# Kernel tuning notes

Hardware: AMD Instinct MI355X
Metric: run time of the kernel (lower is better)

The kernel has to match this reference:

```python
import jax, jax.numpy as jnp
import numpy as np

T = 16384      # trajectory length
Z = 8          # num_zones
DIN = 8        # person_attrs_dim
E = 16         # num edges
PENALTY = 1000.0
DIFFUSION_STRENGTH = 0.2
EPS = 1e-20


def setup_inputs() -> dict:
    key = jax.random.key(0)
    ks = jax.random.split(key, 20)
    s = 0.05  # weight scale
    return {
        "person_attrs": jax.random.normal(ks[0], (DIN,), jnp.float32),
        "times": jnp.arange(T, dtype=jnp.float32),
        "gumbel_u": jax.random.uniform(ks[1], (T, Z), jnp.float32),
        "edge_index": jax.random.randint(ks[2], (2, E), 0, Z),
        "W1": jax.random.normal(ks[3], (256, DIN + 1 + Z), jnp.float32) * s,
        "b1": jnp.zeros((256,), jnp.float32),
        "W2": jax.random.normal(ks[4], (128, 256), jnp.float32) * s,
        "b2": jnp.zeros((128,), jnp.float32),
        "W3": jax.random.normal(ks[5], (64, 128), jnp.float32) * s,
        "b3": jnp.zeros((64,), jnp.float32),
        "W4": jax.random.normal(ks[6], (Z, 64), jnp.float32) * s,
        "b4": jnp.zeros((Z,), jnp.float32),
        "D1": jax.random.normal(ks[7], (128, DIN + 1), jnp.float32) * s,
        "d1": jnp.zeros((128,), jnp.float32),
        "D2": jax.random.normal(ks[8], (64, 128), jnp.float32) * s,
        "d2": jnp.zeros((64,), jnp.float32),
        "D3": jax.random.normal(ks[9], (Z, 64), jnp.float32) * s,
        "d3": jnp.zeros((Z,), jnp.float32),
        "tau": jnp.asarray(1.0, jnp.float32),
    }


def _adjacency(edge_index, num_zones):
    A = jnp.zeros((num_zones, num_zones), jnp.float32)
    A = A.at[edge_index[0], edge_index[1]].set(1.0)
    A = A.at[edge_index[1], edge_index[0]].set(1.0)
    d = jnp.arange(num_zones)
    return A.at[d, d].set(1.0)


def _forward(person_attrs, times, gumbel_u, W1, b1, W2, b2, W3, b3, W4, b4,
             D1, d1, D2, d2, D3, d3, tau, edge_index):
    num_zones = W4.shape[0]
    din = person_attrs.shape[0]
    A = _adjacency(edge_index, num_zones)

    # normalized time: times / times[-1] if times[-1] > 0 else 0
    last = times[-1]
    denom = jnp.where(last > 0, last, jnp.asarray(1.0, times.dtype))
    norm_t = jnp.where(last > 0, times / denom, jnp.zeros_like(times))  # [T]

    # Precompute (attrs, time)-dependent parts batched over all timesteps.
    # trajectory_net layer 1 split: columns [0:din]=attrs, [din]=time, [din+1:]=zone one-hot
    f_base = person_attrs @ W1[:, :din].T + norm_t[:, None] * W1[:, din][None, :] + b1  # [T,256]
    W1z = W1[:, din + 1:]  # [256, Z]

    # diversity_net depends only on (attrs, time): batch it fully.
    h = jax.nn.relu(person_attrs @ D1[:, :din].T + norm_t[:, None] * D1[:, din][None, :] + d1)  # [T,128]
    h = jax.nn.relu(h @ D2.T + d2)                                                              # [T,64]
    diversity = jnp.tanh(h @ D3.T + d3)                                                         # [T,Z]

    gumbels = -jnp.log(-jnp.log(gumbel_u + EPS) + EPS)  # [T,Z]

    zone0 = jax.nn.one_hot(0, num_zones, dtype=jnp.float32)

    def step(zone_soft, xs):
        f1, dv, g = xs
        h1 = jax.nn.relu(f1 + W1z @ zone_soft)
        h2 = jax.nn.relu(W2 @ h1 + b2)
        h3 = jax.nn.relu(W3 @ h2 + b3)
        base_logits = W4 @ h3 + b4
        combined = base_logits + DIFFUSION_STRENGTH * dv
        cur = jnp.argmax(zone_soft)
        constrained = combined - PENALTY * (1.0 - A[cur])
        y = jax.nn.softmax((constrained + g) / tau)
        nxt = jnp.argmax(y)
        hard = jax.nn.one_hot(nxt, num_zones, dtype=y.dtype)
        zone_next = y + jax.lax.stop_gradient(hard - y)  # straight-through hard gumbel
        return zone_next, (constrained, nxt)

    _, (traj_logits, traj_zones) = jax.lax.scan(step, zone0, (f_base, diversity, gumbels))
    return traj_logits, traj_zones


def reference(person_attrs, times, gumbel_u, edge_index, W1, b1, W2, b2, W3, b3,
              W4, b4, D1, d1, D2, d2, D3, d3, tau):
    return _forward(person_attrs, times, gumbel_u, W1, b1, W2, b2, W3, b3, W4, b4,
                    D1, d1, D2, d2, D3, d3, tau, edge_index)
```

## Files before the change

kernel.cpp:

```cpp
#include <hip/hip_runtime.h>
#include <cstdint>

#define T_STEPS 16384

#define WS_U     0
#define WS_V     256
#define WS_W1ZT  512
#define WS_PEN   2560
#define WS_A     2624
#define WS_W4T   2688
#define WS_W2T   3968
#define WS_W3T   36736
#define WS_DV    53120
#define WS_G     184192
#define WS_CONS  315264
#define WS_ABT   1363840
#define WS_A4LR  1888128
#define WS_H3LR  1920896
#define WS_END_F 2183040
#define WSB_NXT8 ((size_t)WS_END_F * 4)
#define WSB_CUR  (WSB_NXT8 + 131072)
#define WSB_CRX  (WSB_CUR + 65536)

#define PB_DIV   0
#define PB_W2T   256
#define PB_W3T   (PB_W2T + 128)
#define PB_GUM   (PB_W3T + 32)
#define PB_SETUP (PB_GUM + 512)
#define NB_PREP  (PB_SETUP + 1)

__device__ __forceinline__ unsigned int fn_compose(unsigned int hi, unsigned int lo) {
  unsigned int r = 0;
  #pragma unroll
  for (int x = 0; x < 8; ++x) {
    unsigned int m = (lo >> (3 * x)) & 7u;
    r |= ((hi >> (3 * m)) & 7u) << (3 * x);
  }
  return r;
}

__global__ void __launch_bounds__(256) k_prepdiv(
    const float* __restrict__ pa, const float* __restrict__ times,
    const float* __restrict__ gum, const int* __restrict__ edge,
    const float* __restrict__ W1, const float* __restrict__ b1,
    const float* __restrict__ W2, const float* __restrict__ W3,
    const float* __restrict__ W4,
    const float* __restrict__ D1, const float* __restrict__ d1,
    const float* __restrict__ D2, const float* __restrict__ d2,
    const float* __restrict__ D3, const float* __restrict__ d3,
    float* __restrict__ ws) {
  __shared__ float sD2[64 * 128];
  __shared__ float sudc[128], svdc[128];
  __shared__ float part[3][8][64];
  int b = blockIdx.x, tid = threadIdx.x;
  if (b < PB_W2T) {
    int lane = tid & 63;
    int w = __builtin_amdgcn_readfirstlane(tid >> 6);
    int t = b * 64 + lane;
    float last = times[T_STEPS - 1];
    float st = (last > 0.0f) ? times[t] / last : 0.0f;
    #pragma unroll
    for (int i = 0; i < 8; ++i)
      ((float4*)sD2)[i * 256 + tid] = ((const float4*)D2)[i * 256 + tid];
    if (tid < 128) {
      float acc = d1[tid];
      #pragma unroll
      for (int i = 0; i < 8; ++i) acc = fmaf(pa[i], D1[tid * 9 + i], acc);
      sudc[tid] = acc;
      svdc[tid] = D1[tid * 9 + 8];
    }
    __syncthreads();
    int j0 = __builtin_amdgcn_readfirstlane(w * 16);
    float accj[16];
    #pragma unroll
    for (int jj = 0; jj < 16; ++jj) accj[jj] = d2[j0 + jj];
    #pragma unroll 4
    for (int k = 0; k < 128; ++k) {
      float h1 = fmaxf(fmaf(st, svdc[k], sudc[k]), 0.0f);
      #pragma unroll
      for (int jj = 0; jj < 16; ++jj)
        accj[jj] = fmaf(sD2[(j0 + jj) * 128 + k], h1, accj[jj]);
    }
    float dvp[8];
    #pragma unroll
    for (int z = 0; z < 8; ++z) dvp[z] = (w == 0) ? d3[z] : 0.0f;
    #pragma unroll
    for (int jj = 0; jj < 16; ++jj) {
      float h2 = fmaxf(accj[jj], 0.0f);
      #pragma unroll
      for (int z = 0; z < 8; ++z)
        dvp[z] = fmaf(D3[z * 64 + j0 + jj], h2, dvp[z]);
    }
    if (w > 0) {
      #pragma unroll
      for (int z = 0; z < 8; ++z) part[w - 1][z][lane] = dvp[z];
    }
    __syncthreads();
    if (w == 0) {
      #pragma unroll
      for (int z = 0; z < 8; ++z) {
        float dvv = dvp[z] + part[0][z][lane] + part[1][z][lane] + part[2][z][lane];
        ws[WS_DV + t * 8 + z] = tanhf(dvv);
      }
    }
  } else if (b < PB_W3T) {
    int e = (b - PB_W2T) * 256 + tid;
    int k = e >> 7, j = e & 127;
    ws[WS_W2T + e] = W2[j * 256 + k];
  } else if (b < PB_GUM) {
    int e = (b - PB_W3T) * 256 + tid;
    int i = e & 63, j = e >> 6;
    ws[WS_W3T + e] = W3[i * 128 + j];
  } else if (b < PB_SETUP) {
    int e = (b - PB_GUM) * 256 + tid;
    float uu = gum[e];
    ws[WS_G + e] = -logf(-logf(uu + 1e-20f) + 1e-20f);
  } else {
    {
      int k = tid;
      float acc = b1[k];
      #pragma unroll
      for (int i = 0; i < 8; ++i) acc = fmaf(pa[i], W1[k * 17 + i], acc);
      ws[WS_U + k] = acc;
      ws[WS_V + k] = W1[k * 17 + 8];
    }
    for (int e = tid; e < 2048; e += 256) {
      int cc = e >> 8, k = e & 255;
      ws[WS_W1ZT + e] = W1[k * 17 + 9 + cc];
    }
    for (int e = tid; e < 512; e += 256) {
      int k = e >> 3, z = e & 7;
      ws[WS_W4T + e] = W4[z * 64 + k];
    }
    if (tid < 64) ws[WS_A + tid] = ((tid >> 3) == (tid & 7)) ? 1.0f : 0.0f;
    __syncthreads();
    if (tid == 0) {
      for (int e = 0; e < 16; ++e) {
        int aa = edge[e], bb = edge[16 + e];
        ws[WS_A + aa * 8 + bb] = 1.0f;
        ws[WS_A + bb * 8 + aa] = 1.0f;
      }
    }
    __syncthreads();
    if (tid < 64) ws[WS_PEN + tid] = 1000.0f * (1.0f - ws[WS_A + tid]);
  }
}

__global__ void __launch_bounds__(256) k_ab4(
    const float* __restrict__ times,
    const float* __restrict__ u_, const float* __restrict__ v_,
    const float* __restrict__ w1zt, const float* __restrict__ w2t,
    const float* __restrict__ w3t, const float* __restrict__ w4t,
    const float* __restrict__ b2, const float* __restrict__ b3,
    const float* __restrict__ b4,
    float* __restrict__ abt, int* __restrict__ crx,
    float* __restrict__ a4lr, float* __restrict__ h3lr) {
  __shared__ float s_au[256], s_av[256];
  __shared__ float s_pa[128], s_pb[128];
  __shared__ unsigned long long s_bal[4];
  __shared__ float s_h2L[128], s_h2R[128];
  __shared__ float s_h3pL[4][64], s_h3pR[4][64];
  __shared__ float s_h3L[64], s_h3R[64];
  __shared__ int s_d2, s_d3, s_cnt;
  int blk = blockIdx.x;
  int c = blk >> 8, tile = blk & 255;
  int tid = threadIdx.x;
  float last = times[T_STEPS - 1];
  float stL = (last > 0.0f) ? times[tile * 64] / last : 0.0f;
  float stR = (last > 0.0f) ? times[tile * 64 + 63] / last : 0.0f;
  {
    float uk = u_[tid] + w1zt[c * 256 + tid];
    float vk = v_[tid];
    float valL = fmaf(stL, vk, uk);
    float valR = fmaf(stR, vk, uk);
    float mn = fminf(valL, valR);
    float mx = fmaxf(valL, valR);
    bool act = (mn > 0.0f);
    bool cross = (!act) && (mx > 0.0f);
    s_au[tid] = act ? uk : 0.0f;
    s_av[tid] = act ? vk : 0.0f;
    unsigned long long bal = __ballot(cross);
    if ((tid & 63) == 0) s_bal[tid >> 6] = bal;
  }
  if (tid == 0) { s_d2 = 0; s_d3 = 0; }
  __syncthreads();
  if (tid == 0) {
    int cnt = 0;
    int list8[8];
    #pragma unroll
    for (int i = 0; i < 8; ++i) list8[i] = 0;
    #pragma unroll
    for (int w = 0; w < 4; ++w) {
      unsigned long long m = s_bal[w];
      while (m) {
        int bit = __ffsll(m) - 1;
        if (cnt < 8) list8[cnt] = w * 64 + bit;
        ++cnt;
        m &= (m - 1);
      }
    }
    crx[blk * 12] = cnt;
    s_cnt = cnt;
    #pragma unroll
    for (int i = 0; i < 8; ++i) crx[blk * 12 + 1 + i] = list8[i];
  }
  {
    int j = tid & 127, half = tid >> 7;
    float A = 0.0f, B = 0.0f;
    const float* wrow = w2t + half * 128 * 128 + j;
    int kb = half * 128;
    #pragma unroll 4
    for (int kk = 0; kk < 128; ++kk) {
      float w = wrow[kk * 128];
      A = fmaf(s_au[kb + kk], w, A);
      B = fmaf(s_av[kb + kk], w, B);
    }
    if (half == 1) { s_pa[j] = A; s_pb[j] = B; }
    __syncthreads();
    if (half == 0) {
      float Af = A + s_pa[j] + b2[j];
      float Bf = B + s_pb[j];
      abt[(size_t)blk * 256 + j * 2]     = Af;
      abt[(size_t)blk * 256 + j * 2 + 1] = Bf;
      float preL = fmaf(stL, Bf, Af);
      float preR = fmaf(stR, Bf, Af);
      if ((preL > 0.0f) != (preR > 0.0f)) atomicOr(&s_d2, 1);
      s_h2L[j] = fmaxf(preL, 0.0f);
      s_h2R[j] = fmaxf(preR, 0.0f);
    }
  }
  __syncthreads();
  {
    int i = tid & 63, jq = tid >> 6;
    float aL = (jq == 0) ? b3[i] : 0.0f;
    float aR = aL;
    int j0 = jq * 32;
    #pragma unroll 4
    for (int jj = 0; jj < 32; ++jj) {
      float w = w3t[(j0 + jj) * 64 + i];
      aL = fmaf(w, s_h2L[j0 + jj], aL);
      aR = fmaf(w, s_h2R[j0 + jj], aR);
    }
    s_h3pL[jq][i] = aL;
    s_h3pR[jq][i] = aR;
  }
  __syncthreads();
  if (tid < 64) {
    float preL = s_h3pL[0][tid] + s_h3pL[1][tid] + s_h3pL[2][tid] + s_h3pL[3][tid];
    float preR = s_h3pR[0][tid] + s_h3pR[1][tid] + s_h3pR[2][tid] + s_h3pR[3][tid];
    if ((preL > 0.0f) != (preR > 0.0f)) atomicOr(&s_d3, 1);
    s_h3L[tid] = fmaxf(preL, 0.0f);
    s_h3R[tid] = fmaxf(preR, 0.0f);
    h3lr[(size_t)blk * 128 + tid]      = preL;
    h3lr[(size_t)blk * 128 + 64 + tid] = preR;
  }
  __syncthreads();
  if (tid < 8) {
    float aL = b4[tid], aR = b4[tid];
    #pragma unroll 8
    for (int i = 0; i < 64; ++i) {
      float w = w4t[i * 8 + tid];
      aL = fmaf(w, s_h3L[i], aL);
      aR = fmaf(w, s_h3R[i], aR);
    }
    a4lr[blk * 16 + tid]     = aL;
    a4lr[blk * 16 + 8 + tid] = aR;
  }
  if (tid == 0) {
    int flag = 0;
    if (s_cnt == 0 && s_d2 == 0) flag = s_d3 ? 2 : 1;
    crx[blk * 12 + 9] = flag;
  }
}

__global__ void __launch_bounds__(256, 8) k_mlp(
    const float* __restrict__ times,
    const float* __restrict__ u_, const float* __restrict__ v_,
    const float* __restrict__ w1zt, const float* __restrict__ w2t,
    const float* __restrict__ abt, const int* __restrict__ crx,
    const float* __restrict__ a4lr, const float* __restrict__ h3lr,
    const float* __restrict__ w3t, const float* __restrict__ w4t,
    const float* __restrict__ b2, const float* __restrict__ b3,
    const float* __restrict__ b4,
    const float* __restrict__ dv, const float* __restrict__ gt,
    const float* __restrict__ pen, const float* __restrict__ tau,
    float* __restrict__ cons_out, unsigned char* __restrict__ nxt_out) {
  __shared__ float part[3][8][64];
  int tid = threadIdx.x;
  int lane = tid & 63;
  int iq = __builtin_amdgcn_readfirstlane(tid >> 6);
  int blk = blockIdx.x;
  int c = blk >> 8, tgrp = blk & 255;
  int t = tgrp * 64 + lane;
  int abase = blk * 256;
  int cbase = blk * 12;
  int flag = crx[cbase + 9];

  if (flag == 1) {
    if (iq == 0) {
      float frac = (float)lane * (1.0f / 63.0f);
      float a4[8];
      #pragma unroll
      for (int z = 0; z < 8; ++z) {
        float L = a4lr[blk * 16 + z];
        float R = a4lr[blk * 16 + 8 + z];
        a4[z] = fmaf(frac, R - L, L);
      }
      float4 dv0 = *(const float4*)(dv + (size_t)t * 8);
      float4 dv1 = *(const float4*)(dv + (size_t)t * 8 + 4);
      float4 g0  = *(const float4*)(gt + (size_t)t * 8);
      float4 g1  = *(const float4*)(gt + (size_t)t * 8 + 4);
      float dvv[8] = {dv0.x, dv0.y, dv0.z, dv0.w, dv1.x, dv1.y, dv1.z, dv1.w};
      float gv[8]  = {g0.x, g0.y, g0.z, g0.w, g1.x, g1.y, g1.z, g1.w};
      float sgn = (tau[0] > 0.0f) ? 1.0f : -1.0f;
      float cons[8];
      float best = 0.0f; int bz = 0;
      #pragma unroll
      for (int z = 0; z < 8; ++z) {
        float lg = fmaf(0.2f, dvv[z], a4[z]) - pen[c * 8 + z];
        cons[z] = lg;
        float yv = (lg + gv[z]) * sgn;
        if (z == 0) { best = yv; bz = 0; }
        else if (yv > best) { best = yv; bz = z; }
      }
      float* co = cons_out + ((size_t)t * 8 + c) * 8;
      *(float4*)co = make_float4(cons[0], cons[1], cons[2], cons[3]);
      *(float4*)(co + 4) = make_float4(cons[4], cons[5], cons[6], cons[7]);
      nxt_out[t * 8 + c] = (unsigned char)bz;
    }
    return;
  }

  float last = times[T_STEPS - 1];
  float st = (last > 0.0f) ? times[t] / last : 0.0f;
  const float* w1c = w1zt + c * 256;
  int cnt = crx[cbase];

  float acc[16];
  if (flag == 2) {
    float frac = (float)lane * (1.0f / 63.0f);
    #pragma unroll
    for (int i = 0; i < 16; ++i) {
      float L = h3lr[(size_t)blk * 128 + iq * 16 + i];
      float R = h3lr[(size_t)blk * 128 + 64 + iq * 16 + i];
      acc[i] = fmaf(frac, R - L, L);
    }
  } else {
    #pragma unroll
    for (int i = 0; i < 16; ++i) acc[i] = b3[iq * 16 + i];
    const float* w3 = w3t + iq * 16;

    if (cnt == 0) {
      #pragma unroll 4
      for (int j = 0; j < 128; ++j) {
        float A = abt[abase + j * 2];
        float B = abt[abase + j * 2 + 1];
        float h2 = fmaxf(fmaf(st, B, A), 0.0f);
        #pragma unroll
        for (int i = 0; i < 16; ++i)
          acc[i] = fmaf(w3[j * 64 + i], h2, acc[i]);
      }
    } else if (cnt <= 8) {
      int kk[8];
      #pragma unroll
      for (int i = 0; i < 8; ++i) kk[i] = (i < cnt) ? crx[cbase + 1 + i] : 0;
      float hx[8];
      #pragma unroll
      for (int i = 0; i < 8; ++i)
        hx[i] = (i < cnt) ? fmaxf(fmaf(st, v_[kk[i]], u_[kk[i]] + w1c[kk[i]]), 0.0f) : 0.0f;
      #pragma unroll 2
      for (int j = 0; j < 128; ++j) {
        float A = abt[abase + j * 2];
        float B = abt[abase + j * 2 + 1];
        float h2p = fmaf(st, B, A);
        #pragma unroll
        for (int i = 0; i < 8; ++i)
          h2p = fmaf(hx[i], w2t[kk[i] * 128 + j], h2p);
        float h2 = fmaxf(h2p, 0.0f);
        #pragma unroll
        for (int i = 0; i < 16; ++i)
          acc[i] = fmaf(w3[j * 64 + i], h2, acc[i]);
      }
    } else {
      for (int j = 0; j < 128; ++j) {
        float h2p = b2[j];
        for (int k = 0; k < 256; ++k) {
          float h1 = fmaxf(fmaf(st, v_[k], u_[k] + w1c[k]), 0.0f);
          h2p = fmaf(w2t[k * 128 + j], h1, h2p);
        }
        float h2 = fmaxf(h2p, 0.0f);
        #pragma unroll
        for (int i = 0; i < 16; ++i)
          acc[i] = fmaf(w3[j * 64 + i], h2, acc[i]);
      }
    }
  }

  float p[8];
  #pragma unroll
  for (int z = 0; z < 8; ++z) p[z] = (iq == 0) ? b4[z] : 0.0f;
  #pragma unroll 4
  for (int i = 0; i < 16; ++i) {
    float h3 = fmaxf(acc[i], 0.0f);
    #pragma unroll
    for (int z = 0; z < 8; ++z)
      p[z] = fmaf(w4t[(iq * 16 + i) * 8 + z], h3, p[z]);
  }
  if (iq > 0) {
    #pragma unroll
    for (int z = 0; z < 8; ++z) part[iq - 1][z][lane] = p[z];
  }
  __syncthreads();
  if (iq == 0) {
    float a4[8];
    #pragma unroll
    for (int z = 0; z < 8; ++z)
      a4[z] = p[z] + part[0][z][lane] + part[1][z][lane] + part[2][z][lane];
    float4 dv0 = *(const float4*)(dv + (size_t)t * 8);
    float4 dv1 = *(const float4*)(dv + (size_t)t * 8 + 4);
    float4 g0  = *(const float4*)(gt + (size_t)t * 8);
    float4 g1  = *(const float4*)(gt + (size_t)t * 8 + 4);
    float dvv[8] = {dv0.x, dv0.y, dv0.z, dv0.w, dv1.x, dv1.y, dv1.z, dv1.w};
    float gv[8]  = {g0.x, g0.y, g0.z, g0.w, g1.x, g1.y, g1.z, g1.w};
    float sgn = (tau[0] > 0.0f) ? 1.0f : -1.0f;
    float cons[8];
    float best = 0.0f; int bz = 0;
    #pragma unroll
    for (int z = 0; z < 8; ++z) {
      float lg = fmaf(0.2f, dvv[z], a4[z]) - pen[c * 8 + z];
      cons[z] = lg;
      float yv = (lg + gv[z]) * sgn;
      if (z == 0) { best = yv; bz = 0; }
      else if (yv > best) { best = yv; bz = z; }
    }
    float* co = cons_out + ((size_t)t * 8 + c) * 8;
    *(float4*)co = make_float4(cons[0], cons[1], cons[2], cons[3]);
    *(float4*)(co + 4) = make_float4(cons[4], cons[5], cons[6], cons[7]);
    nxt_out[t * 8 + c] = (unsigned char)bz;
  }
}

__global__ void __launch_bounds__(1024) k_phaseC(float* __restrict__ ws, float* __restrict__ d_out) {
  int tid = threadIdx.x;
  const unsigned char* nxt8 = (const unsigned char*)ws + WSB_NXT8;
  unsigned int* cur_arr = (unsigned int*)((char*)ws + WSB_CUR);
  const unsigned int IDENT = 0x00FAC688u;
  unsigned int f[16];
  int t0 = tid * 16;
  unsigned int F = IDENT;
  #pragma unroll
  for (int i = 0; i < 16; ++i) {
    uint2 b = *(const uint2*)(nxt8 + (size_t)(t0 + i) * 8);
    unsigned int fn = 0;
    #pragma unroll
    for (int q = 0; q < 4; ++q) fn |= ((b.x >> (8 * q)) & 7u) << (3 * q);
    #pragma unroll
    for (int q = 0; q < 4; ++q) fn |= ((b.y >> (8 * q)) & 7u) << (3 * (q + 4));
    f[i] = fn;
    F = fn_compose(fn, F);
  }
  __shared__ unsigned int sc[1024];
  sc[tid] = F;
  __syncthreads();
  #pragma unroll
  for (int d = 1; d < 1024; d <<= 1) {
    unsigned int v = sc[tid];
    unsigned int p = (tid >= d) ? sc[tid - d] : 0u;
    unsigned int nv = (tid >= d) ? fn_compose(v, p) : v;
    __syncthreads();
    sc[tid] = nv;
    __syncthreads();
  }
  unsigned int E = (tid == 0) ? IDENT : sc[tid - 1];
  unsigned int state = E & 7u;
  #pragma unroll
  for (int i = 0; i < 16; ++i) {
    int tt = t0 + i;
    cur_arr[tt] = state;
    unsigned int nx = (f[i] >> (3 * state)) & 7u;
    d_out[131072 + tt] = (float)nx;
    state = nx;
  }
}

__global__ void k_gather(const float* __restrict__ ws, float* __restrict__ d_out) {
  int idx = blockIdx.x * 256 + threadIdx.x;
  const unsigned int* cur_arr = (const unsigned int*)((const char*)ws + WSB_CUR);
  int t = idx >> 3, z = idx & 7;
  unsigned int cur = cur_arr[t];
  d_out[idx] = ws[WS_CONS + (t * 8 + (int)cur) * 8 + z];
}

extern "C" void kernel_launch(void* const* d_in, const int* in_sizes, int n_in,
                              void* d_out, int out_size, void* d_ws, size_t ws_size,
                              hipStream_t stream) {
  const float* pa    = (const float*)d_in[0];
  const float* times = (const float*)d_in[1];
  const float* gum   = (const float*)d_in[2];
  const int*   edge  = (const int*)d_in[3];
  const float* W1  = (const float*)d_in[4];
  const float* b1  = (const float*)d_in[5];
  const float* W2  = (const float*)d_in[6];
  const float* b2  = (const float*)d_in[7];
  const float* W3  = (const float*)d_in[8];
  const float* b3  = (const float*)d_in[9];
  const float* W4  = (const float*)d_in[10];
  const float* b4  = (const float*)d_in[11];
  const float* D1  = (const float*)d_in[12];
  const float* d1v = (const float*)d_in[13];
  const float* D2  = (const float*)d_in[14];
  const float* d2v = (const float*)d_in[15];
  const float* D3  = (const float*)d_in[16];
  const float* d3v = (const float*)d_in[17];
  const float* tau = (const float*)d_in[18];
  float* ws = (float*)d_ws;
  float* out = (float*)d_out;
  int* crx = (int*)((char*)d_ws + WSB_CRX);

  k_prepdiv<<<NB_PREP, 256, 0, stream>>>(pa, times, gum, edge, W1, b1, W2, W3, W4,
                                         D1, d1v, D2, d2v, D3, d3v, ws);
  k_ab4<<<2048, 256, 0, stream>>>(times, ws + WS_U, ws + WS_V, ws + WS_W1ZT,
                                  ws + WS_W2T, ws + WS_W3T, ws + WS_W4T,
                                  b2, b3, b4, ws + WS_ABT, crx,
                                  ws + WS_A4LR, ws + WS_H3LR);
  k_mlp<<<2048, 256, 0, stream>>>(times, ws + WS_U, ws + WS_V, ws + WS_W1ZT,
                                  ws + WS_W2T, ws + WS_ABT, crx,
                                  ws + WS_A4LR, ws + WS_H3LR,
                                  ws + WS_W3T, ws + WS_W4T, b2, b3, b4,
                                  ws + WS_DV, ws + WS_G, ws + WS_PEN, tau,
                                  ws + WS_CONS, (unsigned char*)ws + WSB_NXT8);
  k_phaseC<<<1, 1024, 0, stream>>>(ws, out);
  k_gather<<<512, 256, 0, stream>>>(ws, out);
}
```

Baseline: 86.49 us.

## Handle tiles with few layer-2 ReLU crossings by interpolation plus sparse correction

Each tile's precompute now records which layer-2 units change ReLU sign within the 64-step tile, using a wave ballot in place of the shared atomic flag. Tiles with no layer-1 crossings and at most eight layer-2 crossings take a new path (flag 3). That path linearly interpolates the layer-3 pre-activation and adds exact corrections only for the crossing units, so they skip the full 128-wide layer-2 loop. The per-block metadata stride grows from 12 to 24 ints, which relies on the workspace region being large enough. It also adds an extra barrier and serial list building in the precompute kernel.

```diff
diff --git a/kernel.cpp b/kernel.cpp
--- a/kernel.cpp
+++ b/kernel.cpp
@@ -158,10 +158,11 @@
   __shared__ float s_au[256], s_av[256];
   __shared__ float s_pa[128], s_pb[128];
   __shared__ unsigned long long s_bal[4];
+  __shared__ unsigned long long s_bal2[2];
   __shared__ float s_h2L[128], s_h2R[128];
   __shared__ float s_h3pL[4][64], s_h3pR[4][64];
   __shared__ float s_h3L[64], s_h3R[64];
-  __shared__ int s_d2, s_d3, s_cnt;
+  __shared__ int s_d3, s_cnt, s_cnt2;
   int blk = blockIdx.x;
   int c = blk >> 8, tile = blk & 255;
   int tid = threadIdx.x;
@@ -182,7 +183,7 @@
     unsigned long long bal = __ballot(cross);
     if ((tid & 63) == 0) s_bal[tid >> 6] = bal;
   }
-  if (tid == 0) { s_d2 = 0; s_d3 = 0; }
+  if (tid == 0) s_d3 = 0;
   __syncthreads();
   if (tid == 0) {
     int cnt = 0;
@@ -199,10 +200,10 @@
         m &= (m - 1);
       }
     }
-    crx[blk * 12] = cnt;
+    crx[blk * 24] = cnt;
     s_cnt = cnt;
     #pragma unroll
-    for (int i = 0; i < 8; ++i) crx[blk * 12 + 1 + i] = list8[i];
+    for (int i = 0; i < 8; ++i) crx[blk * 24 + 1 + i] = list8[i];
   }
   {
     int j = tid & 127, half = tid >> 7;
@@ -217,6 +218,7 @@
     }
     if (half == 1) { s_pa[j] = A; s_pb[j] = B; }
     __syncthreads();
+    bool jcross = false;
     if (half == 0) {
       float Af = A + s_pa[j] + b2[j];
       float Bf = B + s_pb[j];
@@ -224,10 +226,33 @@
       abt[(size_t)blk * 256 + j * 2 + 1] = Bf;
       float preL = fmaf(stL, Bf, Af);
       float preR = fmaf(stR, Bf, Af);
-      if ((preL > 0.0f) != (preR > 0.0f)) atomicOr(&s_d2, 1);
+      jcross = (preL > 0.0f) != (preR > 0.0f);
       s_h2L[j] = fmaxf(preL, 0.0f);
       s_h2R[j] = fmaxf(preR, 0.0f);
     }
+    unsigned long long bal2 = __ballot(jcross);
+    if ((tid & 63) == 0 && tid < 128) s_bal2[tid >> 6] = bal2;
+  }
+  __syncthreads();
+  if (tid == 0) {
+    int cnt2 = 0;
+    int list8[8];
+    #pragma unroll
+    for (int i = 0; i < 8; ++i) list8[i] = 0;
+    #pragma unroll
+    for (int w = 0; w < 2; ++w) {
+      unsigned long long m = s_bal2[w];
+      while (m) {
+        int bit = __ffsll(m) - 1;
+        if (cnt2 < 8) list8[cnt2] = w * 64 + bit;
+        ++cnt2;
+        m &= (m - 1);
+      }
+    }
+    crx[blk * 24 + 10] = cnt2;
+    s_cnt2 = cnt2;
+    #pragma unroll
+    for (int i = 0; i < 8; ++i) crx[blk * 24 + 11 + i] = list8[i];
   }
   __syncthreads();
   {
@@ -267,9 +292,11 @@
     a4lr[blk * 16 + 8 + tid] = aR;
   }
   if (tid == 0) {
-    int flag = 0;
-    if (s_cnt == 0 && s_d2 == 0) flag = s_d3 ? 2 : 1;
-    crx[blk * 12 + 9] = flag;
+    int flag;
+    if (s_cnt > 0 || s_cnt2 > 8) flag = 0;
+    else if (s_cnt2 > 0 || s_d3) flag = 3;
+    else flag = 1;
+    crx[blk * 24 + 9] = flag;
   }
 }
 
@@ -293,7 +320,7 @@
   int c = blk >> 8, tgrp = blk & 255;
   int t = tgrp * 64 + lane;
   int abase = blk * 256;
-  int cbase = blk * 12;
+  int cbase = blk * 24;
   int flag = crx[cbase + 9];
 
   if (flag == 1) {
@@ -335,20 +362,38 @@
   float st = (last > 0.0f) ? times[t] / last : 0.0f;
   const float* w1c = w1zt + c * 256;
   int cnt = crx[cbase];
+  int i0 = iq * 16;
 
   float acc[16];
-  if (flag == 2) {
+  if (flag == 3) {
     float frac = (float)lane * (1.0f / 63.0f);
     #pragma unroll
     for (int i = 0; i < 16; ++i) {
-      float L = h3lr[(size_t)blk * 128 + iq * 16 + i];
-      float R = h3lr[(size_t)blk * 128 + 64 + iq * 16 + i];
+      float L = h3lr[(size_t)blk * 128 + i0 + i];
+      float R = h3lr[(size_t)blk * 128 + 64 + i0 + i];
       acc[i] = fmaf(frac, R - L, L);
     }
+    int cnt2 = crx[cbase + 10];
+    float stL = (last > 0.0f) ? times[tgrp * 64] / last : 0.0f;
+    float stR = (last > 0.0f) ? times[tgrp * 64 + 63] / last : 0.0f;
+    for (int q = 0; q < cnt2; ++q) {
+      int j = crx[cbase + 11 + q];
+      float A = abt[abase + j * 2];
+      float B = abt[abase + j * 2 + 1];
+      float preL = fmaf(stL, B, A);
+      float preR = fmaf(stR, B, A);
+      float rL = fmaxf(preL, 0.0f);
+      float rR = fmaxf(preR, 0.0f);
+      float pre = fmaf(st, B, A);
+      float corr = fmaxf(pre, 0.0f) - fmaf(frac, rR - rL, rL);
+      #pragma unroll
+      for (int i = 0; i < 16; ++i)
+        acc[i] = fmaf(corr, w3t[j * 64 + i0 + i], acc[i]);
+    }
   } else {
     #pragma unroll
-    for (int i = 0; i < 16; ++i) acc[i] = b3[iq * 16 + i];
-    const float* w3 = w3t + iq * 16;
+    for (int i = 0; i < 16; ++i) acc[i] = b3[i0 + i];
+    const float* w3 = w3t + i0;
 
     if (cnt == 0) {
       #pragma unroll 4
@@ -404,7 +449,7 @@
     float h3 = fmaxf(acc[i], 0.0f);
     #pragma unroll
     for (int z = 0; z < 8; ++z)
-      p[z] = fmaf(w4t[(iq * 16 + i) * 8 + z], h3, p[z]);
+      p[z] = fmaf(w4t[(i0 + i) * 8 + z], h3, p[z]);
   }
   if (iq > 0) {
     #pragma unroll
```

Result: faster. 83.21 us (-3.8%).
